# Performance work log

Measured on AMD Instinct MI355X. Metric: run time of the kernel, lower is better.

The kernel has to match this reference:

```python
import jax, jax.numpy as jnp
import numpy as np

HID = 101
IN = 3


def lstm_cell(x, h, c, W_ih, W_hh, b_ih, b_hh):
    # PyTorch LSTMCell gate order: i, f, g, o
    gates = x @ W_ih.T + b_ih + h @ W_hh.T + b_hh  # [B, 4H]
    i, f, g, o = jnp.split(gates, 4, axis=-1)
    i = jax.nn.sigmoid(i)
    f = jax.nn.sigmoid(f)
    g = jnp.tanh(g)
    o = jax.nn.sigmoid(o)
    c_new = f * c + i * g
    h_new = o * jnp.tanh(c_new)
    return h_new, c_new


def setup_inputs() -> dict:
    key = jax.random.key(0)
    ks = jax.random.split(key, 12)
    B, T = 1024, 256
    s1 = 1.0 / np.sqrt(HID)
    u = lambda k, shp: jax.random.uniform(k, shp, jnp.float32, -s1, s1)
    return {
        "input": jax.random.normal(ks[0], (B, T, IN), jnp.float32),
        "W_ih1": u(ks[1], (4 * HID, IN)),
        "W_hh1": u(ks[2], (4 * HID, HID)),
        "b_ih1": u(ks[3], (4 * HID,)),
        "b_hh1": u(ks[4], (4 * HID,)),
        "W_ih2": u(ks[5], (4 * HID, HID)),
        "W_hh2": u(ks[6], (4 * HID, HID)),
        "b_ih2": u(ks[7], (4 * HID,)),
        "b_hh2": u(ks[8], (4 * HID,)),
        "Wl": u(ks[9], (IN, HID)),
        "bl": u(ks[10], (IN,)),
        "future": 32,
    }


def reference(input, W_ih1, W_hh1, b_ih1, b_hh1, W_ih2, W_hh2, b_ih2, b_hh2, Wl, bl, future):
    B = input.shape[0]
    h1 = jnp.zeros((B, HID), input.dtype)
    c1 = jnp.zeros((B, HID), input.dtype)
    h2 = jnp.zeros((B, HID), input.dtype)
    c2 = jnp.zeros((B, HID), input.dtype)

    def step(carry, x_t):
        h1, c1, h2, c2 = carry
        h1, c1 = lstm_cell(x_t, h1, c1, W_ih1, W_hh1, b_ih1, b_hh1)
        h2, c2 = lstm_cell(h1, h2, c2, W_ih2, W_hh2, b_ih2, b_hh2)
        out = h2 @ Wl.T + bl  # [B, 3]
        return (h1, c1, h2, c2), out

    xs = jnp.transpose(input, (1, 0, 2))  # [T, B, 3]
    carry, outs = jax.lax.scan(step, (h1, c1, h2, c2), xs)

    if future > 0:
        last_out = outs[-1]

        def fstep(carry, _):
            h1, c1, h2, c2, out = carry
            h1, c1 = lstm_cell(out, h1, c1, W_ih1, W_hh1, b_ih1, b_hh1)
            h2, c2 = lstm_cell(h1, h2, c2, W_ih2, W_hh2, b_ih2, b_hh2)
            out = h2 @ Wl.T + bl
            return (h1, c1, h2, c2, out), out

        _, fouts = jax.lax.scan(fstep, (*carry, last_out), None, length=future)
        outs = jnp.concatenate([outs, fouts], axis=0)

    return jnp.transpose(outs, (1, 0, 2))  # [B, T+future, 3]
```

## Files before the change

kernel.cpp:

```cpp
#include <hip/hip_runtime.h>
#include <hip/hip_bf16.h>

#define HID 101
#define BATCH 1024
#define RPB 4
#define NBLK 256
#define NTHR 512

#define A1SZ  (7*4*4*512)
#define A2SZ  (7*4*8*512)
#define A2OFF A1SZ
#define AOOFF (A1SZ + A2SZ)
#define AOSZ  (4*512)

typedef _Float16 h8 __attribute__((ext_vector_type(8)));
typedef float f4 __attribute__((ext_vector_type(4)));

__global__ void prep_kernel(const float* __restrict__ W_ih1, const float* __restrict__ W_hh1,
                            const float* __restrict__ b_ih1, const float* __restrict__ b_hh1,
                            const float* __restrict__ W_ih2, const float* __restrict__ W_hh2,
                            const float* __restrict__ b_ih2, const float* __restrict__ b_hh2,
                            const float* __restrict__ Wl, _Float16* __restrict__ wsA) {
    int idx = blockIdx.x * blockDim.x + threadIdx.x;
    int stride = gridDim.x * blockDim.x;
    for (int t = idx; t < A1SZ; t += stride) {
        int i = t & 7, lane = (t >> 3) & 63, kt = (t >> 9) & 3, tau = (t >> 11) & 3, w = t >> 13;
        int k = kt * 32 + ((lane >> 4) & 3) * 8 + i;
        int u = 16 * w + (lane & 15);
        float v = 0.f;
        if (u < HID) {
            int g = tau * HID + u;
            if (k < HID) v = W_hh1[g * HID + k];
            else if (k >= 101 && k <= 103) v = W_ih1[g * 3 + (k - 101)];
            else if (k == 104) v = b_ih1[g] + b_hh1[g];
        }
        wsA[t] = (_Float16)v;
    }
    for (int t = idx; t < A2SZ; t += stride) {
        int i = t & 7, lane = (t >> 3) & 63, kt = (t >> 9) & 7, tau = (t >> 12) & 3, w = t >> 14;
        int k = kt * 32 + ((lane >> 4) & 3) * 8 + i;
        int u = 16 * w + (lane & 15);
        float v = 0.f;
        if (u < HID) {
            int g = tau * HID + u;
            if (k < HID) v = W_ih2[g * HID + k];
            else if (k == 104) v = b_ih2[g] + b_hh2[g];
            else if (k >= 128 && k < 128 + HID) v = W_hh2[g * HID + (k - 128)];
        }
        wsA[A2OFF + t] = (_Float16)v;
    }
    for (int t = idx; t < AOSZ; t += stride) {
        int i = t & 7, lane = (t >> 3) & 63, kt = (t >> 9) & 3;
        int k = kt * 32 + ((lane >> 4) & 3) * 8 + i;
        int j = lane & 15;
        float v = (j < 3 && k < HID) ? Wl[j * HID + k] : 0.f;
        wsA[AOOFF + t] = (_Float16)v;
    }
}

__device__ __forceinline__ float sigm(float z) {
    return __builtin_amdgcn_rcpf(1.f + __expf(-z));
}
__device__ __forceinline__ float tanhf_(float z) {
    return 1.f - 2.f * __builtin_amdgcn_rcpf(__expf(2.f * z) + 1.f);
}

#define KEEP(x) { f4 _kv = __builtin_bit_cast(f4, x); asm volatile("" : "+v"(_kv)); \
                  x = __builtin_bit_cast(h8, _kv); }

__global__ __launch_bounds__(NTHR, 2) void lstm_kernel(
    const float* __restrict__ input, const _Float16* __restrict__ wsA,
    const float* __restrict__ bl, int T, int steps, float* __restrict__ out)
{
    const int tid = threadIdx.x;
    const int wid = tid >> 6, lane = tid & 63;
    const int q = lane >> 4, col = lane & 15;
    const int r0 = blockIdx.x * RPB;
    const int ostride = steps * 3;

    __shared__ _Float16 Hb[2][2048];
    __shared__ _Float16 K2b[2][2048];
    __shared__ float zw[7][4][4][16];

    h8 A1[4][4];
    h8 A2[4][8];
    if (wid < 7) {
        #pragma unroll
        for (int tau = 0; tau < 4; tau++) {
            #pragma unroll
            for (int kt = 0; kt < 4; kt++) {
                A1[tau][kt] = *(const h8*)(wsA + (size_t)(((wid * 4 + tau) * 4 + kt) * 64 + lane) * 8);
                KEEP(A1[tau][kt]);
            }
            #pragma unroll
            for (int kt = 0; kt < 8; kt++) {
                A2[tau][kt] = *(const h8*)(wsA + (size_t)A2OFF + (size_t)(((wid * 4 + tau) * 8 + kt) * 64 + lane) * 8);
                KEEP(A2[tau][kt]);
            }
        }
    } else {
        #pragma unroll
        for (int kt = 0; kt < 4; kt++) {
            A2[0][kt] = *(const h8*)(wsA + (size_t)AOOFF + (size_t)(kt * 64 + lane) * 8);
            KEEP(A2[0][kt]);
        }
    }
    const float bl0 = bl[0], bl1 = bl[1], bl2 = bl[2];

    const int r_ew = lane & 3, ul = lane >> 2;
    const int u = 16 * wid + ul;
    const bool ewv = (wid < 7) && (u < HID);
    const int hslot = (((u >> 5) * 4 + ((u >> 3) & 3)) * 16 + r_ew) * 8 + (u & 7);
    const int boff = (q * 16 + col) * 8;
    const int xr = lane / 3, xj = lane - 3 * xr;
    const int xoff = ((12 + 0) * 16 + xr) * 8 + 5 + xj;

    for (int i2 = tid; i2 < 2048; i2 += NTHR) {
        Hb[0][i2] = (_Float16)0.f; Hb[1][i2] = (_Float16)0.f;
        K2b[0][i2] = (_Float16)0.f; K2b[1][i2] = (_Float16)0.f;
    }
    __syncthreads();
    if (tid < 16) {
        Hb[0][((12 + 1) * 16 + tid) * 8] = (_Float16)1.0f;
        Hb[1][((12 + 1) * 16 + tid) * 8] = (_Float16)1.0f;
    }
    if (tid < 12) {
        int r = tid / 3, j = tid - 3 * (tid / 3);
        float v = input[(size_t)(r0 + r) * T * 3 + j];
        Hb[1][((12 + 0) * 16 + r) * 8 + 5 + j] = (_Float16)v;
    }
    float c1 = 0.f, c2 = 0.f;
    __syncthreads();

    auto STEP = [&](int t, _Float16* Hrd, _Float16* Hwr, _Float16* K2rd, _Float16* K2wr, bool fut) {
        float xv = 0.f;
        if (fut) {
            if (wid == 7) {
                f4 ao = {0.f, 0.f, 0.f, 0.f};
                #pragma unroll
                for (int kt = 0; kt < 4; kt++) {
                    h8 b = *(const h8*)(K2rd + kt * 512 + boff);
                    ao = __builtin_amdgcn_mfma_f32_16x16x32_f16(A2[0][kt], b, ao, 0, 0, 0);
                }
                if (lane < 4) {
                    float o0 = ao[0] + bl0, o1 = ao[1] + bl1, o2 = ao[2] + bl2;
                    float* op = out + (size_t)(r0 + lane) * ostride + (size_t)(t - 1) * 3;
                    op[0] = o0; op[1] = o1; op[2] = o2;
                    Hrd[(12 * 16 + lane) * 8 + 5] = (_Float16)o0;
                    Hrd[(12 * 16 + lane) * 8 + 6] = (_Float16)o1;
                    Hrd[(12 * 16 + lane) * 8 + 7] = (_Float16)o2;
                }
            }
            __syncthreads();
        }
        if (wid < 7) {
            f4 acc0 = {0.f,0.f,0.f,0.f}, acc1 = acc0, acc2 = acc0, acc3 = acc0;
            #pragma unroll
            for (int kt = 0; kt < 4; kt++) {
                h8 b = *(const h8*)(Hrd + kt * 512 + boff);
                acc0 = __builtin_amdgcn_mfma_f32_16x16x32_f16(A1[0][kt], b, acc0, 0, 0, 0);
                acc1 = __builtin_amdgcn_mfma_f32_16x16x32_f16(A1[1][kt], b, acc1, 0, 0, 0);
                acc2 = __builtin_amdgcn_mfma_f32_16x16x32_f16(A1[2][kt], b, acc2, 0, 0, 0);
                acc3 = __builtin_amdgcn_mfma_f32_16x16x32_f16(A1[3][kt], b, acc3, 0, 0, 0);
            }
            if (col < 4) {
                *(f4*)&zw[wid][0][col][4 * q] = acc0;
                *(f4*)&zw[wid][1][col][4 * q] = acc1;
                *(f4*)&zw[wid][2][col][4 * q] = acc2;
                *(f4*)&zw[wid][3][col][4 * q] = acc3;
            }
            float z0 = zw[wid][0][r_ew][ul], z1 = zw[wid][1][r_ew][ul];
            float z2 = zw[wid][2][r_ew][ul], z3 = zw[wid][3][r_ew][ul];
            float ig = sigm(z0), fg = sigm(z1), gg = tanhf_(z2), og = sigm(z3);
            c1 = fg * c1 + ig * gg;
            float h1v = og * tanhf_(c1);
            if (ewv) Hwr[hslot] = (_Float16)h1v;
        } else {
            if (!fut) {
                if (t > 0) {
                    f4 ao = {0.f, 0.f, 0.f, 0.f};
                    #pragma unroll
                    for (int kt = 0; kt < 4; kt++) {
                        h8 b = *(const h8*)(K2rd + kt * 512 + boff);
                        ao = __builtin_amdgcn_mfma_f32_16x16x32_f16(A2[0][kt], b, ao, 0, 0, 0);
                    }
                    if (lane < 4) {
                        float* op = out + (size_t)(r0 + lane) * ostride + (size_t)(t - 1) * 3;
                        op[0] = ao[0] + bl0; op[1] = ao[1] + bl1; op[2] = ao[2] + bl2;
                    }
                }
                if (t + 1 < T && lane < 12)
                    xv = input[(size_t)(r0 + xr) * T * 3 + (size_t)(t + 1) * 3 + xj];
            }
        }
        __syncthreads();
        if (wid < 7) {
            f4 acc0 = {0.f,0.f,0.f,0.f}, acc1 = acc0, acc2 = acc0, acc3 = acc0;
            #pragma unroll
            for (int kt = 0; kt < 4; kt++) {
                h8 b = *(const h8*)(Hwr + kt * 512 + boff);
                acc0 = __builtin_amdgcn_mfma_f32_16x16x32_f16(A2[0][kt], b, acc0, 0, 0, 0);
                acc1 = __builtin_amdgcn_mfma_f32_16x16x32_f16(A2[1][kt], b, acc1, 0, 0, 0);
                acc2 = __builtin_amdgcn_mfma_f32_16x16x32_f16(A2[2][kt], b, acc2, 0, 0, 0);
                acc3 = __builtin_amdgcn_mfma_f32_16x16x32_f16(A2[3][kt], b, acc3, 0, 0, 0);
            }
            #pragma unroll
            for (int kt = 0; kt < 4; kt++) {
                h8 b = *(const h8*)(K2rd + kt * 512 + boff);
                acc0 = __builtin_amdgcn_mfma_f32_16x16x32_f16(A2[0][kt + 4], b, acc0, 0, 0, 0);
                acc1 = __builtin_amdgcn_mfma_f32_16x16x32_f16(A2[1][kt + 4], b, acc1, 0, 0, 0);
                acc2 = __builtin_amdgcn_mfma_f32_16x16x32_f16(A2[2][kt + 4], b, acc2, 0, 0, 0);
                acc3 = __builtin_amdgcn_mfma_f32_16x16x32_f16(A2[3][kt + 4], b, acc3, 0, 0, 0);
            }
            if (col < 4) {
                *(f4*)&zw[wid][0][col][4 * q] = acc0;
                *(f4*)&zw[wid][1][col][4 * q] = acc1;
                *(f4*)&zw[wid][2][col][4 * q] = acc2;
                *(f4*)&zw[wid][3][col][4 * q] = acc3;
            }
            float z0 = zw[wid][0][r_ew][ul], z1 = zw[wid][1][r_ew][ul];
            float z2 = zw[wid][2][r_ew][ul], z3 = zw[wid][3][r_ew][ul];
            float ig = sigm(z0), fg = sigm(z1), gg = tanhf_(z2), og = sigm(z3);
            c2 = fg * c2 + ig * gg;
            float h2v = og * tanhf_(c2);
            if (ewv) K2wr[hslot] = (_Float16)h2v;
        } else {
            if (!fut && t + 1 < T && lane < 12)
                Hwr[xoff] = (_Float16)xv;
        }
        __syncthreads();
    };

    for (int t = 0; t < T; t += 2) {
        STEP(t,     Hb[1], Hb[0], K2b[1], K2b[0], false);
        STEP(t + 1, Hb[0], Hb[1], K2b[0], K2b[1], false);
    }
    for (int t = T; t < steps; t += 2) {
        STEP(t,     Hb[1], Hb[0], K2b[1], K2b[0], true);
        STEP(t + 1, Hb[0], Hb[1], K2b[0], K2b[1], true);
    }
    if (wid == 7) {
        f4 ao = {0.f, 0.f, 0.f, 0.f};
        #pragma unroll
        for (int kt = 0; kt < 4; kt++) {
            h8 b = *(const h8*)(&K2b[1][0] + kt * 512 + boff);
            ao = __builtin_amdgcn_mfma_f32_16x16x32_f16(A2[0][kt], b, ao, 0, 0, 0);
        }
        if (lane < 4) {
            float* op = out + (size_t)(r0 + lane) * ostride + (size_t)(steps - 1) * 3;
            op[0] = ao[0] + bl0; op[1] = ao[1] + bl1; op[2] = ao[2] + bl2;
        }
    }
}

extern "C" void kernel_launch(void* const* d_in, const int* in_sizes, int n_in,
                              void* d_out, int out_size, void* d_ws, size_t ws_size,
                              hipStream_t stream) {
    const float* input = (const float*)d_in[0];
    const float* W_ih1 = (const float*)d_in[1];
    const float* W_hh1 = (const float*)d_in[2];
    const float* b_ih1 = (const float*)d_in[3];
    const float* b_hh1 = (const float*)d_in[4];
    const float* W_ih2 = (const float*)d_in[5];
    const float* W_hh2 = (const float*)d_in[6];
    const float* b_ih2 = (const float*)d_in[7];
    const float* b_hh2 = (const float*)d_in[8];
    const float* Wl    = (const float*)d_in[9];
    const float* bl    = (const float*)d_in[10];
    int T = in_sizes[0] / (BATCH * 3);
    int steps = out_size / (BATCH * 3);
    _Float16* wsA = (_Float16*)d_ws;

    hipLaunchKernelGGL(prep_kernel, dim3(512), dim3(256), 0, stream,
                       W_ih1, W_hh1, b_ih1, b_hh1, W_ih2, W_hh2, b_ih2, b_hh2, Wl, wsA);
    hipLaunchKernelGGL(lstm_kernel, dim3(NBLK), dim3(NTHR), 0, stream,
                       input, wsA, bl, T, steps, (float*)d_out);
}
```

Before: 481.5 us.

## Pin weights in AGPRs, swizzle LDS state layout, load only live batch columns

Weight fragments are now forced into accumulator registers (AGPRs) through inline asm constraints with scheduling barriers, which frees VGPRs at the two-blocks-per-CU occupancy target. The shared-memory layout of the h/x/bias buffers is rotated per quad (column index offset by 4*q) to spread LDS bank accesses. B-fragment loads are predicated to the 4 real batch columns, with the other lanes feeding zeros. The asm constraint trick and the layout changes have to stay consistent across the writers, the bias and input slots, and the readers.

```diff
diff --git a/kernel.cpp b/kernel.cpp
--- a/kernel.cpp
+++ b/kernel.cpp
@@ -65,9 +65,6 @@
     return 1.f - 2.f * __builtin_amdgcn_rcpf(__expf(2.f * z) + 1.f);
 }
 
-#define KEEP(x) { f4 _kv = __builtin_bit_cast(f4, x); asm volatile("" : "+v"(_kv)); \
-                  x = __builtin_bit_cast(h8, _kv); }
-
 __global__ __launch_bounds__(NTHR, 2) void lstm_kernel(
     const float* __restrict__ input, const _Float16* __restrict__ wsA,
     const float* __restrict__ bl, int T, int steps, float* __restrict__ out)
@@ -82,27 +79,29 @@
     __shared__ _Float16 K2b[2][2048];
     __shared__ float zw[7][4][4][16];
 
-    h8 A1[4][4];
-    h8 A2[4][8];
+    h8 A1r[4][4], A2r[4][8];
     if (wid < 7) {
         #pragma unroll
         for (int tau = 0; tau < 4; tau++) {
             #pragma unroll
             for (int kt = 0; kt < 4; kt++) {
-                A1[tau][kt] = *(const h8*)(wsA + (size_t)(((wid * 4 + tau) * 4 + kt) * 64 + lane) * 8);
-                KEEP(A1[tau][kt]);
+                h8 w = *(const h8*)(wsA + (size_t)(((wid * 4 + tau) * 4 + kt) * 64 + lane) * 8);
+                asm volatile("" : "=a"(A1r[tau][kt]) : "0"(w));
+                __builtin_amdgcn_sched_barrier(0);
             }
             #pragma unroll
             for (int kt = 0; kt < 8; kt++) {
-                A2[tau][kt] = *(const h8*)(wsA + (size_t)A2OFF + (size_t)(((wid * 4 + tau) * 8 + kt) * 64 + lane) * 8);
-                KEEP(A2[tau][kt]);
+                h8 w = *(const h8*)(wsA + (size_t)A2OFF + (size_t)(((wid * 4 + tau) * 8 + kt) * 64 + lane) * 8);
+                asm volatile("" : "=a"(A2r[tau][kt]) : "0"(w));
+                __builtin_amdgcn_sched_barrier(0);
             }
         }
     } else {
         #pragma unroll
         for (int kt = 0; kt < 4; kt++) {
-            A2[0][kt] = *(const h8*)(wsA + (size_t)AOOFF + (size_t)(kt * 64 + lane) * 8);
-            KEEP(A2[0][kt]);
+            h8 w = *(const h8*)(wsA + (size_t)AOOFF + (size_t)(kt * 64 + lane) * 8);
+            asm volatile("" : "=a"(A2r[0][kt]) : "0"(w));
+            __builtin_amdgcn_sched_barrier(0);
         }
     }
     const float bl0 = bl[0], bl1 = bl[1], bl2 = bl[2];
@@ -110,10 +109,11 @@
     const int r_ew = lane & 3, ul = lane >> 2;
     const int u = 16 * wid + ul;
     const bool ewv = (wid < 7) && (u < HID);
-    const int hslot = (((u >> 5) * 4 + ((u >> 3) & 3)) * 16 + r_ew) * 8 + (u & 7);
-    const int boff = (q * 16 + col) * 8;
+    const int qfu = (u >> 3) & 3;
+    const int hslot = (((u >> 5) * 4 + qfu) * 16 + ((r_ew + 4 * qfu) & 15)) * 8 + (u & 7);
+    const int boff = (q * 16 + ((col + 4 * q) & 15)) * 8;
     const int xr = lane / 3, xj = lane - 3 * xr;
-    const int xoff = ((12 + 0) * 16 + xr) * 8 + 5 + xj;
+    const int xoff = (12 * 16 + xr) * 8 + 5 + xj;
 
     for (int i2 = tid; i2 < 2048; i2 += NTHR) {
         Hb[0][i2] = (_Float16)0.f; Hb[1][i2] = (_Float16)0.f;
@@ -121,13 +121,13 @@
     }
     __syncthreads();
     if (tid < 16) {
-        Hb[0][((12 + 1) * 16 + tid) * 8] = (_Float16)1.0f;
-        Hb[1][((12 + 1) * 16 + tid) * 8] = (_Float16)1.0f;
+        int p = (tid + 4) & 15;
+        Hb[0][(13 * 16 + p) * 8] = (_Float16)1.0f;
+        Hb[1][(13 * 16 + p) * 8] = (_Float16)1.0f;
     }
     if (tid < 12) {
         int r = tid / 3, j = tid - 3 * (tid / 3);
-        float v = input[(size_t)(r0 + r) * T * 3 + j];
-        Hb[1][((12 + 0) * 16 + r) * 8 + 5 + j] = (_Float16)v;
+        Hb[1][(12 * 16 + r) * 8 + 5 + j] = (_Float16)input[(size_t)(r0 + r) * T * 3 + j];
     }
     float c1 = 0.f, c2 = 0.f;
     __syncthreads();
@@ -139,8 +139,9 @@
                 f4 ao = {0.f, 0.f, 0.f, 0.f};
                 #pragma unroll
                 for (int kt = 0; kt < 4; kt++) {
-                    h8 b = *(const h8*)(K2rd + kt * 512 + boff);
-                    ao = __builtin_amdgcn_mfma_f32_16x16x32_f16(A2[0][kt], b, ao, 0, 0, 0);
+                    h8 b = (_Float16)0.f;
+                    if (col < 4) b = *(const h8*)(K2rd + kt * 512 + boff);
+                    ao = __builtin_amdgcn_mfma_f32_16x16x32_f16(A2r[0][kt], b, ao, 0, 0, 0);
                 }
                 if (lane < 4) {
                     float o0 = ao[0] + bl0, o1 = ao[1] + bl1, o2 = ao[2] + bl2;
@@ -157,11 +158,12 @@
             f4 acc0 = {0.f,0.f,0.f,0.f}, acc1 = acc0, acc2 = acc0, acc3 = acc0;
             #pragma unroll
             for (int kt = 0; kt < 4; kt++) {
-                h8 b = *(const h8*)(Hrd + kt * 512 + boff);
-                acc0 = __builtin_amdgcn_mfma_f32_16x16x32_f16(A1[0][kt], b, acc0, 0, 0, 0);
-                acc1 = __builtin_amdgcn_mfma_f32_16x16x32_f16(A1[1][kt], b, acc1, 0, 0, 0);
-                acc2 = __builtin_amdgcn_mfma_f32_16x16x32_f16(A1[2][kt], b, acc2, 0, 0, 0);
-                acc3 = __builtin_amdgcn_mfma_f32_16x16x32_f16(A1[3][kt], b, acc3, 0, 0, 0);
+                h8 b = (_Float16)0.f;
+                if (col < 4) b = *(const h8*)(Hrd + kt * 512 + boff);
+                acc0 = __builtin_amdgcn_mfma_f32_16x16x32_f16(A1r[0][kt], b, acc0, 0, 0, 0);
+                acc1 = __builtin_amdgcn_mfma_f32_16x16x32_f16(A1r[1][kt], b, acc1, 0, 0, 0);
+                acc2 = __builtin_amdgcn_mfma_f32_16x16x32_f16(A1r[2][kt], b, acc2, 0, 0, 0);
+                acc3 = __builtin_amdgcn_mfma_f32_16x16x32_f16(A1r[3][kt], b, acc3, 0, 0, 0);
             }
             if (col < 4) {
                 *(f4*)&zw[wid][0][col][4 * q] = acc0;
@@ -181,8 +183,9 @@
                     f4 ao = {0.f, 0.f, 0.f, 0.f};
                     #pragma unroll
                     for (int kt = 0; kt < 4; kt++) {
-                        h8 b = *(const h8*)(K2rd + kt * 512 + boff);
-                        ao = __builtin_amdgcn_mfma_f32_16x16x32_f16(A2[0][kt], b, ao, 0, 0, 0);
+                        h8 b = (_Float16)0.f;
+                        if (col < 4) b = *(const h8*)(K2rd + kt * 512 + boff);
+                        ao = __builtin_amdgcn_mfma_f32_16x16x32_f16(A2r[0][kt], b, ao, 0, 0, 0);
                     }
                     if (lane < 4) {
                         float* op = out + (size_t)(r0 + lane) * ostride + (size_t)(t - 1) * 3;
@@ -198,19 +201,21 @@
             f4 acc0 = {0.f,0.f,0.f,0.f}, acc1 = acc0, acc2 = acc0, acc3 = acc0;
             #pragma unroll
             for (int kt = 0; kt < 4; kt++) {
-                h8 b = *(const h8*)(Hwr + kt * 512 + boff);
-                acc0 = __builtin_amdgcn_mfma_f32_16x16x32_f16(A2[0][kt], b, acc0, 0, 0, 0);
-                acc1 = __builtin_amdgcn_mfma_f32_16x16x32_f16(A2[1][kt], b, acc1, 0, 0, 0);
-                acc2 = __builtin_amdgcn_mfma_f32_16x16x32_f16(A2[2][kt], b, acc2, 0, 0, 0);
-                acc3 = __builtin_amdgcn_mfma_f32_16x16x32_f16(A2[3][kt], b, acc3, 0, 0, 0);
-            }
-            #pragma unroll
-            for (int kt = 0; kt < 4; kt++) {
-                h8 b = *(const h8*)(K2rd + kt * 512 + boff);
-                acc0 = __builtin_amdgcn_mfma_f32_16x16x32_f16(A2[0][kt + 4], b, acc0, 0, 0, 0);
-                acc1 = __builtin_amdgcn_mfma_f32_16x16x32_f16(A2[1][kt + 4], b, acc1, 0, 0, 0);
-                acc2 = __builtin_amdgcn_mfma_f32_16x16x32_f16(A2[2][kt + 4], b, acc2, 0, 0, 0);
-                acc3 = __builtin_amdgcn_mfma_f32_16x16x32_f16(A2[3][kt + 4], b, acc3, 0, 0, 0);
+                h8 b = (_Float16)0.f;
+                if (col < 4) b = *(const h8*)(Hwr + kt * 512 + boff);
+                acc0 = __builtin_amdgcn_mfma_f32_16x16x32_f16(A2r[0][kt], b, acc0, 0, 0, 0);
+                acc1 = __builtin_amdgcn_mfma_f32_16x16x32_f16(A2r[1][kt], b, acc1, 0, 0, 0);
+                acc2 = __builtin_amdgcn_mfma_f32_16x16x32_f16(A2r[2][kt], b, acc2, 0, 0, 0);
+                acc3 = __builtin_amdgcn_mfma_f32_16x16x32_f16(A2r[3][kt], b, acc3, 0, 0, 0);
+            }
+            #pragma unroll
+            for (int kt = 0; kt < 4; kt++) {
+                h8 b = (_Float16)0.f;
+                if (col < 4) b = *(const h8*)(K2rd + kt * 512 + boff);
+                acc0 = __builtin_amdgcn_mfma_f32_16x16x32_f16(A2r[0][kt + 4], b, acc0, 0, 0, 0);
+                acc1 = __builtin_amdgcn_mfma_f32_16x16x32_f16(A2r[1][kt + 4], b, acc1, 0, 0, 0);
+                acc2 = __builtin_amdgcn_mfma_f32_16x16x32_f16(A2r[2][kt + 4], b, acc2, 0, 0, 0);
+                acc3 = __builtin_amdgcn_mfma_f32_16x16x32_f16(A2r[3][kt + 4], b, acc3, 0, 0, 0);
             }
             if (col < 4) {
                 *(f4*)&zw[wid][0][col][4 * q] = acc0;
@@ -243,8 +248,9 @@
         f4 ao = {0.f, 0.f, 0.f, 0.f};
         #pragma unroll
         for (int kt = 0; kt < 4; kt++) {
-            h8 b = *(const h8*)(&K2b[1][0] + kt * 512 + boff);
-            ao = __builtin_amdgcn_mfma_f32_16x16x32_f16(A2[0][kt], b, ao, 0, 0, 0);
+            h8 b = (_Float16)0.f;
+            if (col < 4) b = *(const h8*)(&K2b[1][0] + kt * 512 + boff);
+            ao = __builtin_amdgcn_mfma_f32_16x16x32_f16(A2r[0][kt], b, ao, 0, 0, 0);
         }
         if (lane < 4) {
             float* op = out + (size_t)(r0 + lane) * ostride + (size_t)(steps - 1) * 3;
```

New measurement: 511.8 us. 6.3% more time.
